# Kernel optimization log

Hardware: AMD Instinct MI355X
Metric: run time of the kernel (lower is better)

Reference implementation:

```python
import jax, jax.numpy as jnp
import numpy as np

K = 128
NITER = 10


def _sq_dist(x, c):
    x2 = jnp.sum(x * x, axis=1, keepdims=True)          # [N,1]
    c2 = jnp.sum(c * c, axis=1)                          # [K]
    return x2 + c2[None, :] - 2.0 * (x @ c.T)


def _kmeans(x, key):
    N, D = x.shape
    idx = jax.random.permutation(key, N)[:K]             # torch.randperm(N)[:K]
    c0 = x[idx]

    def step(c, _):
        cl = jnp.argmin(_sq_dist(x, c), axis=1)          # nearest assignment [N]
        counts = jax.ops.segment_sum(jnp.ones((N,), x.dtype), cl, num_segments=K)  # bincount
        sums = jax.ops.segment_sum(x, cl, num_segments=K)                          # [K,D] (vectorized over D)
        # c = sums / counts; NaN (empty cluster, 0/0) -> 0, matching c[isnan(c)]=0
        c_new = jnp.where(counts[:, None] > 0, sums / jnp.maximum(counts, 1.0)[:, None], 0.0)
        return c_new, None

    c, _ = jax.lax.scan(step, c0, None, length=NITER)
    return c


def setup_inputs() -> dict:
    key = jax.random.key(0)
    x = jax.random.normal(key, (500000, 64), dtype=jnp.float32)
    return {"x": x}


def reference(x):
    # KMeans runs on x.detach(); forward output has no grad path through centroids
    centroids = _kmeans(jax.lax.stop_gradient(x), jax.random.key(42))
    distances = _sq_dist(x, centroids)                   # [N, K]
    # Faithful to normalize_distance: distances.sum(1, keepdim=True)[0] indexes
    # ROW 0 of the [N,1] row-sums -> a single scalar broadcast to all rows.
    denom = jnp.sum(distances[0])
    probs = 1.0 - distances / denom
    return probs
```

## Files before the change

kernel.cpp:

```cpp
#include <hip/hip_runtime.h>
#include <cstdint>
#include <cstddef>

#define NPTS 500000
#define DIM 64
#define KC 128
#define KM_ITERS 10
#define NGROUPS (NPTS / 32)

typedef __bf16 bf16x8 __attribute__((ext_vector_type(8)));
typedef float f32x4 __attribute__((ext_vector_type(4)));

__device__ __forceinline__ float wave_reduce_add(float v) {
#pragma unroll
  for (int off = 32; off > 0; off >>= 1) v += __shfl_xor(v, off, 64);
  return v;
}

__device__ __forceinline__ bf16x8 cvt8(float4 a, float4 b) {
  bf16x8 r;
  r[0] = (__bf16)a.x; r[1] = (__bf16)a.y; r[2] = (__bf16)a.z; r[3] = (__bf16)a.w;
  r[4] = (__bf16)b.x; r[5] = (__bf16)b.y; r[6] = (__bf16)b.z; r[7] = (__bf16)b.w;
  return r;
}

__global__ void k_cvt(const float* __restrict__ x, bf16x8* __restrict__ xb8) {
  int n = NPTS * DIM / 8;
  for (int i = blockIdx.x * 256 + threadIdx.x; i < n; i += gridDim.x * 256) {
    const float4* xp = (const float4*)(x + (size_t)i * 8);
    xb8[i] = cvt8(xp[0], xp[1]);
  }
}

__global__ void k_initc(const float* __restrict__ x, float* __restrict__ cent,
                        float* __restrict__ c2, float* __restrict__ sums,
                        float* __restrict__ cnts) {
  int k = blockIdx.x, d = threadIdx.x;
  long src = (long)k * 3891 + 7;
  float v = x[src * DIM + d];
  cent[k * DIM + d] = v;
  sums[k * DIM + d] = 0.f;
  float s = wave_reduce_add(v * v);
  if (d == 0) { c2[k] = s; cnts[k] = 0.f; }
}

__global__ void k_update(const float* __restrict__ sums, const float* __restrict__ cnts,
                         float* __restrict__ cent, float* __restrict__ c2,
                         float* __restrict__ sums_z, float* __restrict__ cnts_z) {
  int k = blockIdx.x, d = threadIdx.x;
  float c = cnts[k];
  float v = (c > 0.f) ? (sums[k * DIM + d] / c) : 0.f;
  cent[k * DIM + d] = v;
  sums_z[k * DIM + d] = 0.f;
  float s = wave_reduce_add(v * v);
  if (d == 0) { c2[k] = s; cnts_z[k] = 0.f; }
}

__global__ __launch_bounds__(256, 2)
void k_assign(const __bf16* __restrict__ xb, const float* __restrict__ cent,
              const float* __restrict__ c2, float* __restrict__ sums,
              float* __restrict__ cnts) {
  __shared__ bf16x8 sA[1024];
  __shared__ float4 xT4[4][320];
  __shared__ int4 sm4[4][8];
  __shared__ float ms[4][16][65];
  __shared__ float lc[KC];

  const int lane = threadIdx.x & 63;
  const int wid = threadIdx.x >> 6;
  const int col = lane & 15;
  const int grp = lane >> 4;

  for (int e = threadIdx.x; e < 1024; e += 256) {
    int t = e >> 7, ks = (e >> 6) & 1, l = e & 63;
    const float* cp = cent + (size_t)(t * 16 + (l & 15)) * DIM + ks * 32 + (l >> 4) * 8;
    sA[e] = cvt8(*(const float4*)cp, *(const float4*)(cp + 4));
  }
  for (int i = threadIdx.x; i < KC; i += 256) lc[i] = 0.f;

  float c2s[32];
#pragma unroll
  for (int tt = 0; tt < 8; tt++)
#pragma unroll
    for (int r = 0; r < 4; r++) c2s[tt * 4 + r] = c2[tt * 16 + grp * 4 + r];
#pragma unroll
  for (int i = 0; i < 32; i++) asm volatile("" : "+v"(c2s[i]));

  __syncthreads();

  f32x4 accs[32];
#pragma unroll
  for (int i = 0; i < 32; i++) accs[i] = (f32x4){0.f, 0.f, 0.f, 0.f};

  char* xTw = (char*)&xT4[wid][0];
  int* smw = (int*)&sm4[wid][0];
  const bf16x8* sAp = sA;

  const int nw = gridDim.x * 4;
  for (int g = blockIdx.x * 4 + wid; g < NGROUPS; g += nw) {
    asm volatile("" : "+v"(sAp));
    int n0 = g * 32;
    int mink[2];
#pragma unroll
    for (int h = 0; h < 2; h++) {
      const bf16x8* xr = (const bf16x8*)(xb + (size_t)(n0 + h * 16 + col) * DIM + grp * 8);
      bf16x8 v0 = xr[0];
      bf16x8 v1 = xr[4];

      int slotb = ((((h << 1) | (col >> 3)) ^ grp) & 3) * 16 + (col & 7) * 2;
#pragma unroll
      for (int j = 0; j < 8; j++) {
        *(__bf16*)(xTw + (grp * 8 + j) * 80 + slotb) = v0[j];
        *(__bf16*)(xTw + (32 + grp * 8 + j) * 80 + slotb) = v1[j];
      }

      f32x4 acc[8];
#pragma unroll
      for (int tt = 0; tt < 8; tt++) acc[tt] = (f32x4){0.f, 0.f, 0.f, 0.f};
#pragma unroll
      for (int tt = 0; tt < 8; tt++)
        acc[tt] = __builtin_amdgcn_mfma_f32_16x16x32_bf16(sAp[tt * 128 + lane], v0, acc[tt], 0, 0, 0);
#pragma unroll
      for (int tt = 0; tt < 8; tt++)
        acc[tt] = __builtin_amdgcn_mfma_f32_16x16x32_bf16(sAp[tt * 128 + 64 + lane], v1, acc[tt], 0, 0, 0);

      float minv = 3.4e38f;
      int mk = 0;
#pragma unroll
      for (int tt = 0; tt < 8; tt++)
#pragma unroll
        for (int r = 0; r < 4; r++) {
          float s = fmaf(-2.f, acc[tt][r], c2s[tt * 4 + r]);
          int k = tt * 16 + grp * 4 + r;
          if (s < minv) { minv = s; mk = k; }
        }
#pragma unroll
      for (int off = 16; off <= 32; off <<= 1) {
        float ov = __shfl_xor(minv, off, 64);
        int ok = __shfl_xor(mk, off, 64);
        if (ov < minv || (ov == minv && ok < mk)) { minv = ov; mk = ok; }
      }
      mink[h] = mk;
    }

    if (grp == 0) {
      smw[col] = mink[0];
      smw[16 + col] = mink[1];
      atomicAdd(&lc[mink[0]], 1.f);
      atomicAdd(&lc[mink[1]], 1.f);
    }

    int4 mlo = *(int4*)&smw[grp * 8];
    int4 mhi = *(int4*)&smw[grp * 8 + 4];
    int m0 = mlo.x, m1 = mlo.y, m2 = mlo.z, m3 = mlo.w;
    int m4 = mhi.x, m5 = mhi.y, m6 = mhi.z, m7 = mhi.w;

    bf16x8 xf[4];
#pragma unroll
    for (int dt = 0; dt < 4; dt++) {
      int d = dt * 16 + col;
      int slot = (grp ^ ((d >> 3) & 3)) & 3;
      xf[dt] = *(const bf16x8*)(xTw + d * 80 + slot * 16);
    }

#pragma unroll
    for (int tt = 0; tt < 8; tt++) {
      int c = tt * 16 + col;
      union { unsigned u[4]; bf16x8 v; } oh;
      oh.u[0] = (m0 == c ? 0x3F80u : 0u) | (m1 == c ? 0x3F800000u : 0u);
      oh.u[1] = (m2 == c ? 0x3F80u : 0u) | (m3 == c ? 0x3F800000u : 0u);
      oh.u[2] = (m4 == c ? 0x3F80u : 0u) | (m5 == c ? 0x3F800000u : 0u);
      oh.u[3] = (m6 == c ? 0x3F80u : 0u) | (m7 == c ? 0x3F800000u : 0u);
#pragma unroll
      for (int dt = 0; dt < 4; dt++)
        accs[tt * 4 + dt] = __builtin_amdgcn_mfma_f32_16x16x32_bf16(oh.v, xf[dt], accs[tt * 4 + dt], 0, 0, 0);
    }
  }

  __syncthreads();
#pragma unroll
  for (int tt = 0; tt < 8; tt++) {
#pragma unroll
    for (int dt = 0; dt < 4; dt++)
#pragma unroll
      for (int r = 0; r < 4; r++)
        ms[wid][grp * 4 + r][dt * 16 + col] = accs[tt * 4 + dt][r];
    __syncthreads();
    for (int i = threadIdx.x; i < 1024; i += 256) {
      int row = i >> 6, d = i & 63;
      float s = (ms[0][row][d] + ms[1][row][d]) + (ms[2][row][d] + ms[3][row][d]);
      atomicAdd(&sums[(tt * 16 + row) * DIM + d], s);
    }
    __syncthreads();
  }
  for (int i = threadIdx.x; i < KC; i += 256) atomicAdd(&cnts[i], lc[i]);
}

__global__ void k_denom(const float* __restrict__ x, const float* __restrict__ cent,
                        const float* __restrict__ c2, float* __restrict__ denom) {
  __shared__ float sd[KC];
  int k = threadIdx.x;
  float x2 = 0.f, dot = 0.f;
  for (int d = 0; d < DIM; d++) {
    float xv = x[d];
    x2 = fmaf(xv, xv, x2);
    dot = fmaf(xv, cent[k * DIM + d], dot);
  }
  sd[k] = (x2 + c2[k]) - 2.f * dot;
  __syncthreads();
  if (k == 0) {
    float s = 0.f;
    for (int i = 0; i < KC; i++) s += sd[i];
    denom[0] = s;
  }
}

__global__ __launch_bounds__(256, 2)
void k_probs(const float* __restrict__ x, const float* __restrict__ cent,
             const float* __restrict__ c2, const float* __restrict__ denom,
             float* __restrict__ out) {
  const int lane = threadIdx.x & 63;
  const int wid = threadIdx.x >> 6;
  const int col = lane & 15;
  const int grp = lane >> 4;

  bf16x8 afr[2][8];
  float c2g[32];
#pragma unroll
  for (int t = 0; t < 8; t++) {
    const float* cp = cent + (size_t)(t * 16 + col) * DIM;
#pragma unroll
    for (int ks = 0; ks < 2; ks++) {
      float4 f0 = *(const float4*)(cp + ks * 32 + grp * 8);
      float4 f1 = *(const float4*)(cp + ks * 32 + grp * 8 + 4);
      afr[ks][t] = cvt8(f0, f1);
    }
#pragma unroll
    for (int r = 0; r < 4; r++) c2g[t * 4 + r] = c2[t * 16 + grp * 4 + r];
  }
  float invd = 1.0f / denom[0];

  int w = blockIdx.x * 4 + wid;
  int nw = gridDim.x * 4;
  for (int t = w; t < NPTS / 16; t += nw) {
    int n0 = t * 16;
    const float* xp = x + (size_t)(n0 + col) * DIM;
    float4 a0 = *(const float4*)(xp + grp * 8);
    float4 a1 = *(const float4*)(xp + grp * 8 + 4);
    float4 b0 = *(const float4*)(xp + 32 + grp * 8);
    float4 b1 = *(const float4*)(xp + 32 + grp * 8 + 4);
    bf16x8 xb0 = cvt8(a0, a1), xb1 = cvt8(b0, b1);

    float sq = a0.x * a0.x + a0.y * a0.y + a0.z * a0.z + a0.w * a0.w
             + a1.x * a1.x + a1.y * a1.y + a1.z * a1.z + a1.w * a1.w
             + b0.x * b0.x + b0.y * b0.y + b0.z * b0.z + b0.w * b0.w
             + b1.x * b1.x + b1.y * b1.y + b1.z * b1.z + b1.w * b1.w;
    sq += __shfl_xor(sq, 16, 64);
    sq += __shfl_xor(sq, 32, 64);

    f32x4 acc[8];
#pragma unroll
    for (int tt = 0; tt < 8; tt++) acc[tt] = (f32x4){0.f, 0.f, 0.f, 0.f};
#pragma unroll
    for (int tt = 0; tt < 8; tt++)
      acc[tt] = __builtin_amdgcn_mfma_f32_16x16x32_bf16(afr[0][tt], xb0, acc[tt], 0, 0, 0);
#pragma unroll
    for (int tt = 0; tt < 8; tt++)
      acc[tt] = __builtin_amdgcn_mfma_f32_16x16x32_bf16(afr[1][tt], xb1, acc[tt], 0, 0, 0);

    float* op = out + (size_t)(n0 + col) * KC + grp * 4;
#pragma unroll
    for (int tt = 0; tt < 8; tt++) {
      float4 q;
      q.x = 1.f - ((sq + c2g[tt * 4 + 0]) - 2.f * acc[tt][0]) * invd;
      q.y = 1.f - ((sq + c2g[tt * 4 + 1]) - 2.f * acc[tt][1]) * invd;
      q.z = 1.f - ((sq + c2g[tt * 4 + 2]) - 2.f * acc[tt][2]) * invd;
      q.w = 1.f - ((sq + c2g[tt * 4 + 3]) - 2.f * acc[tt][3]) * invd;
      *(float4*)(op + tt * 16) = q;
    }
  }
}

extern "C" void kernel_launch(void* const* d_in, const int* in_sizes, int n_in,
                              void* d_out, int out_size, void* d_ws, size_t ws_size,
                              hipStream_t stream) {
  const float* x = (const float*)d_in[0];
  float* out = (float*)d_out;

  float* cent = (float*)d_ws;
  float* c2 = cent + KC * DIM;
  float* sums = c2 + KC;
  float* cnts = sums + KC * DIM;
  float* denom = cnts + KC;

  bf16x8* xb8 = (bf16x8*)d_out;
  const __bf16* xb = (const __bf16*)d_out;

  k_cvt<<<2048, 256, 0, stream>>>(x, xb8);
  k_initc<<<KC, DIM, 0, stream>>>(x, cent, c2, sums, cnts);
  for (int it = 0; it < KM_ITERS; it++) {
    k_assign<<<512, 256, 0, stream>>>(xb, cent, c2, sums, cnts);
    k_update<<<KC, DIM, 0, stream>>>(sums, cnts, cent, c2, sums, cnts);
  }
  k_denom<<<1, KC, 0, stream>>>(x, cent, c2, denom);
  k_probs<<<512, 256, 0, stream>>>(x, cent, c2, denom, out);
}
```

Before: 743.1 us.

## Software-pipeline one-hot centroid sums with next group's distance MFMAs and fuse denom into probs

The assign loop now defers the one-hot sum MFMAs for the previous 32-point group so they are issued alongside the loads and distance MFMAs of the current group, and it drains the last group after the loop. The goal is to hide the LDS round-trip and load latency. The distance accumulators start from -0.5*c2 and the loop takes an argmax, which removes the per-element fma. The separate single-block denom kernel is folded into each wave of k_probs, saving a launch at the cost of redundant per-wave work.

```diff
diff --git a/kernel.cpp b/kernel.cpp
--- a/kernel.cpp
+++ b/kernel.cpp
@@ -56,6 +56,54 @@
   if (d == 0) { c2[k] = s; cnts_z[k] = 0.f; }
 }
 
+#define ONEHOT_SUMS(MLO, MHI)                                                  \
+  {                                                                            \
+    int m0 = MLO.x, m1 = MLO.y, m2 = MLO.z, m3 = MLO.w;                        \
+    int m4 = MHI.x, m5 = MHI.y, m6 = MHI.z, m7 = MHI.w;                        \
+    _Pragma("unroll") for (int tt = 0; tt < 8; tt++) {                         \
+      int c = tt * 16 + col;                                                   \
+      union { unsigned u[4]; bf16x8 v; } oh;                                   \
+      oh.u[0] = (m0 == c ? 0x3F80u : 0u) | (m1 == c ? 0x3F800000u : 0u);       \
+      oh.u[1] = (m2 == c ? 0x3F80u : 0u) | (m3 == c ? 0x3F800000u : 0u);       \
+      oh.u[2] = (m4 == c ? 0x3F80u : 0u) | (m5 == c ? 0x3F800000u : 0u);       \
+      oh.u[3] = (m6 == c ? 0x3F80u : 0u) | (m7 == c ? 0x3F800000u : 0u);       \
+      accs[tt * 4 + 0] = __builtin_amdgcn_mfma_f32_16x16x32_bf16(oh.v, xf0, accs[tt * 4 + 0], 0, 0, 0); \
+      accs[tt * 4 + 1] = __builtin_amdgcn_mfma_f32_16x16x32_bf16(oh.v, xf1, accs[tt * 4 + 1], 0, 0, 0); \
+      accs[tt * 4 + 2] = __builtin_amdgcn_mfma_f32_16x16x32_bf16(oh.v, xf2, accs[tt * 4 + 2], 0, 0, 0); \
+      accs[tt * 4 + 3] = __builtin_amdgcn_mfma_f32_16x16x32_bf16(oh.v, xf3, accs[tt * 4 + 3], 0, 0, 0); \
+    }                                                                          \
+  }
+
+#define DIST_H(V0, V1, H, MK)                                                  \
+  {                                                                            \
+    int slotb = (((((H) << 1) | (col >> 3)) ^ grp) & 3) * 16 + (col & 7) * 2;  \
+    _Pragma("unroll") for (int j = 0; j < 8; j++) {                            \
+      *(__bf16*)(xTw + (grp * 8 + j) * 80 + slotb) = V0[j];                    \
+      *(__bf16*)(xTw + (32 + grp * 8 + j) * 80 + slotb) = V1[j];               \
+    }                                                                          \
+    f32x4 acc[8];                                                              \
+    _Pragma("unroll") for (int tt = 0; tt < 8; tt++)                           \
+      acc[tt] = (f32x4){c2h[tt * 4 + 0], c2h[tt * 4 + 1],                      \
+                        c2h[tt * 4 + 2], c2h[tt * 4 + 3]};                     \
+    _Pragma("unroll") for (int tt = 0; tt < 8; tt++)                           \
+      acc[tt] = __builtin_amdgcn_mfma_f32_16x16x32_bf16(sAp[tt * 128 + lane], V0, acc[tt], 0, 0, 0); \
+    _Pragma("unroll") for (int tt = 0; tt < 8; tt++)                           \
+      acc[tt] = __builtin_amdgcn_mfma_f32_16x16x32_bf16(sAp[tt * 128 + 64 + lane], V1, acc[tt], 0, 0, 0); \
+    float maxv = -3.4e38f; int mk = 0;                                         \
+    _Pragma("unroll") for (int tt = 0; tt < 8; tt++)                           \
+      _Pragma("unroll") for (int r = 0; r < 4; r++) {                          \
+        float a = acc[tt][r];                                                  \
+        int k = tt * 16 + grp * 4 + r;                                         \
+        if (a > maxv) { maxv = a; mk = k; }                                    \
+      }                                                                        \
+    _Pragma("unroll") for (int off = 16; off <= 32; off <<= 1) {               \
+      float ov = __shfl_xor(maxv, off, 64);                                    \
+      int ok = __shfl_xor(mk, off, 64);                                        \
+      if (ov > maxv || (ov == maxv && ok < mk)) { maxv = ov; mk = ok; }        \
+    }                                                                          \
+    MK = mk;                                                                   \
+  }
+
 __global__ __launch_bounds__(256, 2)
 void k_assign(const __bf16* __restrict__ xb, const float* __restrict__ cent,
               const float* __restrict__ c2, float* __restrict__ sums,
@@ -78,13 +126,13 @@
   }
   for (int i = threadIdx.x; i < KC; i += 256) lc[i] = 0.f;
 
-  float c2s[32];
+  float c2h[32];
 #pragma unroll
   for (int tt = 0; tt < 8; tt++)
 #pragma unroll
-    for (int r = 0; r < 4; r++) c2s[tt * 4 + r] = c2[tt * 16 + grp * 4 + r];
-#pragma unroll
-  for (int i = 0; i < 32; i++) asm volatile("" : "+v"(c2s[i]));
+    for (int r = 0; r < 4; r++) c2h[tt * 4 + r] = -0.5f * c2[tt * 16 + grp * 4 + r];
+#pragma unroll
+  for (int i = 0; i < 32; i++) asm volatile("" : "+v"(c2h[i]));
 
   __syncthreads();
 
@@ -96,85 +144,51 @@
   int* smw = (int*)&sm4[wid][0];
   const bf16x8* sAp = sA;
 
+  bf16x8 xf0, xf1, xf2, xf3;
+#pragma unroll
+  for (int j = 0; j < 8; j++) { xf0[j] = (__bf16)0.f; }
+  xf1 = xf0; xf2 = xf0; xf3 = xf0;
+  int have_prev = 0;
+
   const int nw = gridDim.x * 4;
   for (int g = blockIdx.x * 4 + wid; g < NGROUPS; g += nw) {
     asm volatile("" : "+v"(sAp));
+
+    int4 mlo = {0, 0, 0, 0}, mhi = {0, 0, 0, 0};
+    if (have_prev) {
+      mlo = *(const int4*)&smw[grp * 8];
+      mhi = *(const int4*)&smw[grp * 8 + 4];
+    }
+
     int n0 = g * 32;
-    int mink[2];
-#pragma unroll
-    for (int h = 0; h < 2; h++) {
-      const bf16x8* xr = (const bf16x8*)(xb + (size_t)(n0 + h * 16 + col) * DIM + grp * 8);
-      bf16x8 v0 = xr[0];
-      bf16x8 v1 = xr[4];
-
-      int slotb = ((((h << 1) | (col >> 3)) ^ grp) & 3) * 16 + (col & 7) * 2;
-#pragma unroll
-      for (int j = 0; j < 8; j++) {
-        *(__bf16*)(xTw + (grp * 8 + j) * 80 + slotb) = v0[j];
-        *(__bf16*)(xTw + (32 + grp * 8 + j) * 80 + slotb) = v1[j];
-      }
-
-      f32x4 acc[8];
-#pragma unroll
-      for (int tt = 0; tt < 8; tt++) acc[tt] = (f32x4){0.f, 0.f, 0.f, 0.f};
-#pragma unroll
-      for (int tt = 0; tt < 8; tt++)
-        acc[tt] = __builtin_amdgcn_mfma_f32_16x16x32_bf16(sAp[tt * 128 + lane], v0, acc[tt], 0, 0, 0);
-#pragma unroll
-      for (int tt = 0; tt < 8; tt++)
-        acc[tt] = __builtin_amdgcn_mfma_f32_16x16x32_bf16(sAp[tt * 128 + 64 + lane], v1, acc[tt], 0, 0, 0);
-
-      float minv = 3.4e38f;
-      int mk = 0;
-#pragma unroll
-      for (int tt = 0; tt < 8; tt++)
-#pragma unroll
-        for (int r = 0; r < 4; r++) {
-          float s = fmaf(-2.f, acc[tt][r], c2s[tt * 4 + r]);
-          int k = tt * 16 + grp * 4 + r;
-          if (s < minv) { minv = s; mk = k; }
-        }
-#pragma unroll
-      for (int off = 16; off <= 32; off <<= 1) {
-        float ov = __shfl_xor(minv, off, 64);
-        int ok = __shfl_xor(mk, off, 64);
-        if (ov < minv || (ov == minv && ok < mk)) { minv = ov; mk = ok; }
-      }
-      mink[h] = mk;
-    }
+    const bf16x8* xr0 = (const bf16x8*)(xb + (size_t)(n0 + col) * DIM + grp * 8);
+    const bf16x8* xr1 = (const bf16x8*)(xb + (size_t)(n0 + 16 + col) * DIM + grp * 8);
+    bf16x8 v0a = xr0[0], v1a = xr0[4];
+    bf16x8 v0b = xr1[0], v1b = xr1[4];
+
+    if (have_prev) ONEHOT_SUMS(mlo, mhi);
+
+    int mk0, mk1;
+    DIST_H(v0a, v1a, 0, mk0);
+    DIST_H(v0b, v1b, 1, mk1);
 
     if (grp == 0) {
-      smw[col] = mink[0];
-      smw[16 + col] = mink[1];
-      atomicAdd(&lc[mink[0]], 1.f);
-      atomicAdd(&lc[mink[1]], 1.f);
-    }
-
-    int4 mlo = *(int4*)&smw[grp * 8];
-    int4 mhi = *(int4*)&smw[grp * 8 + 4];
-    int m0 = mlo.x, m1 = mlo.y, m2 = mlo.z, m3 = mlo.w;
-    int m4 = mhi.x, m5 = mhi.y, m6 = mhi.z, m7 = mhi.w;
-
-    bf16x8 xf[4];
-#pragma unroll
-    for (int dt = 0; dt < 4; dt++) {
-      int d = dt * 16 + col;
-      int slot = (grp ^ ((d >> 3) & 3)) & 3;
-      xf[dt] = *(const bf16x8*)(xTw + d * 80 + slot * 16);
-    }
-
-#pragma unroll
-    for (int tt = 0; tt < 8; tt++) {
-      int c = tt * 16 + col;
-      union { unsigned u[4]; bf16x8 v; } oh;
-      oh.u[0] = (m0 == c ? 0x3F80u : 0u) | (m1 == c ? 0x3F800000u : 0u);
-      oh.u[1] = (m2 == c ? 0x3F80u : 0u) | (m3 == c ? 0x3F800000u : 0u);
-      oh.u[2] = (m4 == c ? 0x3F80u : 0u) | (m5 == c ? 0x3F800000u : 0u);
-      oh.u[3] = (m6 == c ? 0x3F80u : 0u) | (m7 == c ? 0x3F800000u : 0u);
-#pragma unroll
-      for (int dt = 0; dt < 4; dt++)
-        accs[tt * 4 + dt] = __builtin_amdgcn_mfma_f32_16x16x32_bf16(oh.v, xf[dt], accs[tt * 4 + dt], 0, 0, 0);
-    }
+      smw[col] = mk0;
+      smw[16 + col] = mk1;
+      atomicAdd(&lc[mk0], 1.f);
+      atomicAdd(&lc[mk1], 1.f);
+    }
+
+    { int d = 0 * 16 + col; int s = (grp ^ ((d >> 3) & 3)) & 3; xf0 = *(const bf16x8*)(xTw + d * 80 + s * 16); }
+    { int d = 1 * 16 + col; int s = (grp ^ ((d >> 3) & 3)) & 3; xf1 = *(const bf16x8*)(xTw + d * 80 + s * 16); }
+    { int d = 2 * 16 + col; int s = (grp ^ ((d >> 3) & 3)) & 3; xf2 = *(const bf16x8*)(xTw + d * 80 + s * 16); }
+    { int d = 3 * 16 + col; int s = (grp ^ ((d >> 3) & 3)) & 3; xf3 = *(const bf16x8*)(xTw + d * 80 + s * 16); }
+    have_prev = 1;
+  }
+  if (have_prev) {
+    int4 mlo = *(const int4*)&smw[grp * 8];
+    int4 mhi = *(const int4*)&smw[grp * 8 + 4];
+    ONEHOT_SUMS(mlo, mhi);
   }
 
   __syncthreads();
@@ -196,29 +210,9 @@
   for (int i = threadIdx.x; i < KC; i += 256) atomicAdd(&cnts[i], lc[i]);
 }
 
-__global__ void k_denom(const float* __restrict__ x, const float* __restrict__ cent,
-                        const float* __restrict__ c2, float* __restrict__ denom) {
-  __shared__ float sd[KC];
-  int k = threadIdx.x;
-  float x2 = 0.f, dot = 0.f;
-  for (int d = 0; d < DIM; d++) {
-    float xv = x[d];
-    x2 = fmaf(xv, xv, x2);
-    dot = fmaf(xv, cent[k * DIM + d], dot);
-  }
-  sd[k] = (x2 + c2[k]) - 2.f * dot;
-  __syncthreads();
-  if (k == 0) {
-    float s = 0.f;
-    for (int i = 0; i < KC; i++) s += sd[i];
-    denom[0] = s;
-  }
-}
-
 __global__ __launch_bounds__(256, 2)
 void k_probs(const float* __restrict__ x, const float* __restrict__ cent,
-             const float* __restrict__ c2, const float* __restrict__ denom,
-             float* __restrict__ out) {
+             const float* __restrict__ c2, float* __restrict__ out) {
   const int lane = threadIdx.x & 63;
   const int wid = threadIdx.x >> 6;
   const int col = lane & 15;
@@ -238,7 +232,18 @@
 #pragma unroll
     for (int r = 0; r < 4; r++) c2g[t * 4 + r] = c2[t * 16 + grp * 4 + r];
   }
-  float invd = 1.0f / denom[0];
+
+  float c2a = c2[lane], c2b = c2[64 + lane];
+  float x2_0 = 0.f, dA = 0.f, dB = 0.f;
+#pragma unroll 8
+  for (int d = 0; d < DIM; d++) {
+    float xv = x[d];
+    x2_0 = fmaf(xv, xv, x2_0);
+    dA = fmaf(xv, cent[(size_t)lane * DIM + d], dA);
+    dB = fmaf(xv, cent[(size_t)(64 + lane) * DIM + d], dB);
+  }
+  float part = ((x2_0 + c2a) - 2.f * dA) + ((x2_0 + c2b) - 2.f * dB);
+  float invd = 1.0f / wave_reduce_add(part);
 
   int w = blockIdx.x * 4 + wid;
   int nw = gridDim.x * 4;
@@ -291,7 +296,6 @@
   float* c2 = cent + KC * DIM;
   float* sums = c2 + KC;
   float* cnts = sums + KC * DIM;
-  float* denom = cnts + KC;
 
   bf16x8* xb8 = (bf16x8*)d_out;
   const __bf16* xb = (const __bf16*)d_out;
@@ -302,6 +306,5 @@
     k_assign<<<512, 256, 0, stream>>>(xb, cent, c2, sums, cnts);
     k_update<<<KC, DIM, 0, stream>>>(sums, cnts, cent, c2, sums, cnts);
   }
-  k_denom<<<1, KC, 0, stream>>>(x, cent, c2, denom);
-  k_probs<<<512, 256, 0, stream>>>(x, cent, c2, denom, out);
-}
+  k_probs<<<512, 256, 0, stream>>>(x, cent, c2, out);
+}
```

New measurement: 993.7 us. 33.7% more time.
